# Kernel optimization log

Hardware: AMD Instinct MI355X
Metric: run time of the kernel (lower is better)

The kernel has to match this reference:

```python
import jax, jax.numpy as jnp
import numpy as np

K = 5  # Chebyshev order


def laplacian(w):
    # normalized Laplacian: I - D^{-1/2} W D^{-1/2}
    d = jnp.sum(w, axis=1)
    d_re = 1.0 / jnp.sqrt(d + 1e-5)
    return jnp.eye(w.shape[0], dtype=w.dtype) - d_re[:, None] * w * d_re[None, :]


def cheb_terms(x, lap, k):
    # x: [B,N,C], lap: [N,N] -> [B,k,N,C]
    # Faithful to torch code: T0 = ones, then (x, lap@x) recurrence for k>2.
    t0 = jnp.ones_like(x)
    if k == 1:
        return t0[:, None]
    t1 = jnp.matmul(lap, x)
    if k == 2:
        return jnp.stack([t0, t1], axis=1)
    terms = [t0, x, t1]
    tkm1, tk = x, t1
    for _ in range(3, k):
        tkm1, tk = tk, 2.0 * jnp.matmul(lap, tk) - tkm1
        terms.append(tk)
    return jnp.stack(terms, axis=1)


def graph_conv(x, lap, w, k):
    # torch: cp.permute(0,2,3,1).flatten(2) @ w, i.e. flat index = c*k + t
    t = cheb_terms(x, lap, k)                       # [B,k,N,C]
    C = x.shape[-1]
    O = w.shape[-1]
    return jnp.einsum('bknc,cko->bno', t, w.reshape(C, k, O))


def setup_inputs() -> dict:
    key = jax.random.key(0)
    ks = jax.random.split(key, 9)
    B, N, Cin, H = 8192, 32, 60, 128
    return {
        'x': jax.random.normal(ks[0], (B, N, Cin), dtype=jnp.float32),
        'adj': jax.random.normal(ks[1], (N, N), dtype=jnp.float32) * 0.1,
        'adj_bias': jax.random.normal(ks[2], (1,), dtype=jnp.float32) * 0.1 + 0.2,
        'w1': jax.random.normal(ks[3], (K * Cin, H), dtype=jnp.float32) * 0.05,
        'b1': jax.random.normal(ks[4], (1, 1, H), dtype=jnp.float32) * 0.05,
        'w2': jax.random.normal(ks[5], (K * H, H), dtype=jnp.float32) * 0.05,
        'b2': jax.random.normal(ks[6], (1, 1, H), dtype=jnp.float32) * 0.05,
        'fc_w': jax.random.normal(ks[7], (2, N * H), dtype=jnp.float32) * 0.02,
        'fc_b': jax.random.normal(ks[8], (2,), dtype=jnp.float32) * 0.02,
    }


def reference(x, adj, adj_bias, w1, b1, w2, b2, fc_w, fc_b):
    # DGCNN.forward (eval mode: dropout = identity)
    a = jax.nn.relu(adj + adj_bias)
    lap = laplacian(a)
    h = graph_conv(x, lap, w1, K)
    h = jax.nn.relu(h + b1)      # B1ReLU
    h = graph_conv(h, lap, w2, K)
    h = jax.nn.relu(h + b2)
    h = h.reshape(h.shape[0], -1)  # [B, N*H]
    return h @ fc_w.T + fc_b
```

## Files before the change

### kernel.cpp

```cpp
#include <hip/hip_runtime.h>

typedef unsigned short u16;
typedef unsigned int u32;
typedef short bf16x8 __attribute__((ext_vector_type(8)));
typedef float f32x4 __attribute__((ext_vector_type(4)));

#define MFMA16(a, b, c) __builtin_amdgcn_mfma_f32_16x16x32_bf16((a), (b), (c), 0, 0, 0)

__device__ __forceinline__ u16 f2bf(float f) {
  u32 u = __builtin_bit_cast(u32, f);
  u += 0x7FFFu + ((u >> 16) & 1u);
  return (u16)(u >> 16);
}
__device__ __forceinline__ u32 pk2bf(float a, float b) {
#if __has_builtin(__builtin_amdgcn_cvt_pk_bf16_f32)
  auto v = __builtin_amdgcn_cvt_pk_bf16_f32(a, b);
  return __builtin_bit_cast(u32, v);
#else
  return (u32)f2bf(a) | ((u32)f2bf(b) << 16);
#endif
}

#define WS_MGF   0
#define WS_WT1F  8192
#define WS_WT2F  73728
#define WS_B1    204800
#define WS_B2    205312

__global__ void prep_kernel(const float* __restrict__ adj,
                            const float* __restrict__ adj_bias,
                            const float* __restrict__ w1,
                            const float* __restrict__ b1,
                            const float* __restrict__ w2,
                            const float* __restrict__ b2,
                            char* __restrict__ ws) {
  const int tid = threadIdx.x;
  if (blockIdx.x == 0) {
    __shared__ float sa[1024], Ls[1024], L2s[1024], L3s[1024], sdre[32];
    float bias = adj_bias[0];
    for (int i = tid; i < 1024; i += 256) sa[i] = fmaxf(adj[i] + bias, 0.0f);
    __syncthreads();
    if (tid < 32) {
      float s = 0.0f;
      for (int c = 0; c < 32; ++c) s += sa[tid * 32 + c];
      sdre[tid] = 1.0f / sqrtf(s + 1e-5f);
    }
    __syncthreads();
    for (int i = tid; i < 1024; i += 256) {
      int n = i >> 5, c = i & 31;
      Ls[i] = (n == c ? 1.0f : 0.0f) - sdre[n] * sa[i] * sdre[c];
    }
    __syncthreads();
    for (int i = tid; i < 1024; i += 256) {
      int r = i >> 5, c = i & 31;
      float s = 0.0f;
      for (int m = 0; m < 32; ++m) s += Ls[r * 32 + m] * Ls[m * 32 + c];
      L2s[i] = s;
    }
    __syncthreads();
    for (int i = tid; i < 1024; i += 256) {
      int r = i >> 5, c = i & 31;
      float s = 0.0f;
      for (int m = 0; m < 32; ++m) s += L2s[r * 32 + m] * Ls[m * 32 + c];
      L3s[i] = s;
    }
    __syncthreads();
    u16* MGf = (u16*)(ws + WS_MGF);
    for (int i = tid; i < 4096; i += 256) {
      int jt = i >> 9, lane = (i >> 3) & 63, j = i & 7;
      int col = jt * 16 + (lane & 15);
      int k = ((lane >> 4) << 3) + j;
      int kk = col >> 5, np = col & 31;
      float v;
      if (kk == 0)      v = (np == k) ? 1.0f : 0.0f;
      else if (kk == 1) v = Ls[np * 32 + k];
      else if (kk == 2) v = 2.0f * L2s[np * 32 + k] - (np == k ? 1.0f : 0.0f);
      else              v = 4.0f * L3s[np * 32 + k] - 3.0f * Ls[np * 32 + k];
      MGf[i] = f2bf(v);
    }
    float* B1 = (float*)(ws + WS_B1);
    float* B2 = (float*)(ws + WS_B2);
    if (tid < 128) {
      float s = b1[tid];
      for (int c = 0; c < 60; ++c) s += w1[(c * 5) * 128 + tid];
      B1[tid] = s;
    } else {
      int o = tid - 128;
      float s = b2[o];
      for (int c = 0; c < 128; ++c) s += w2[(c * 5) * 128 + o];
      B2[o] = s;
    }
  } else {
    u16* WT1F = (u16*)(ws + WS_WT1F);
    u16* WT2F = (u16*)(ws + WS_WT2F);
    int g = (blockIdx.x - 1) * 256 + tid;
    for (int i = g; i < 32768; i += 16 * 256) {
      int j = i & 7, lane = (i >> 3) & 63, ks = (i >> 9) & 3;
      int h = (i >> 11) & 1, ot = i >> 12;
      int q = lane >> 4;
      int c = h * 32 + q * 8 + j;
      int o = ot * 16 + (lane & 15);
      WT1F[i] = (c < 60) ? f2bf(w1[(c * 5 + ks + 1) * 128 + o]) : (u16)0;
    }
    for (int i = g; i < 65536; i += 16 * 256) {
      int j = i & 7, lane = (i >> 3) & 63, ks = (i >> 9) & 3;
      int h = (i >> 11) & 3, mt = i >> 13;
      int q = lane >> 4;
      int c2 = h * 32 + q * 8 + j;
      int o = mt * 16 + (lane & 15);
      WT2F[i] = f2bf(w2[(c2 * 5 + ks + 1) * 128 + o]);
    }
  }
}

__global__ __launch_bounds__(256, 4) void dgcnn_kernel(
    const float* __restrict__ x,
    const char* __restrict__ ws,
    const float* __restrict__ fc_w,
    const float* __restrict__ fc_b,
    float* __restrict__ out) {
  __shared__ __align__(16) char arena[35840];
  __shared__ float red[16];
  u16* XtA = (u16*)arena;
  u16* XtB = (u16*)(arena + 5120);
  u16* HtA = (u16*)arena;
  u16* HtB = (u16*)(arena + 9216);
  u16* YA  = (u16*)(arena + 18432);
  u16* YB  = (u16*)(arena + 27136);

  const u16* MGf  = (const u16*)(ws + WS_MGF);
  const u16* WT1F = (const u16*)(ws + WS_WT1F);
  const u16* WT2F = (const u16*)(ws + WS_WT2F);
  const float* bias1 = (const float*)(ws + WS_B1);
  const float* bias2 = (const float*)(ws + WS_B2);

  const int tid = threadIdx.x;
  const int w = tid >> 6, lane = tid & 63;
  const int l15 = lane & 15, q = lane >> 4;
  const int b0 = blockIdx.x * 2;
  const f32x4 z4 = {0.0f, 0.0f, 0.0f, 0.0f};

  bf16x8 mB0 = *(const bf16x8*)(MGf + ((2 * w + 0) * 64 + lane) * 8);
  bf16x8 mB1 = *(const bf16x8*)(MGf + ((2 * w + 1) * 64 + lane) * 8);

  for (int i = tid; i < 160; i += 256) {
    int r = 60 + i / 40, c = i % 40;
    XtA[r * 40 + c] = 0;
    XtB[r * 40 + c] = 0;
  }
  const float* xb = x + (size_t)b0 * 1920;
  for (int i = tid; i < 1920; i += 256) {
    int n = i / 60, c = i - n * 60;
    u32 p = pk2bf(xb[i], xb[1920 + i]);
    XtA[c * 40 + n] = (u16)p;
    XtB[c * 40 + n] = (u16)(p >> 16);
  }
  __syncthreads();

  f32x4 acc1A[2][2] = {{z4, z4}, {z4, z4}};
  f32x4 acc1B[2][2] = {{z4, z4}, {z4, z4}};
#pragma unroll
  for (int h = 0; h < 2; ++h) {
    {
      f32x4 gA[2][2], gB[2][2];
#pragma unroll
      for (int mtl = 0; mtl < 2; ++mtl) {
        int roff = ((2 * h + mtl) * 16 + l15) * 40 + q * 8;
        bf16x8 aA = *(const bf16x8*)&XtA[roff];
        bf16x8 aB = *(const bf16x8*)&XtB[roff];
        gA[mtl][0] = MFMA16(aA, mB0, z4);
        gA[mtl][1] = MFMA16(aA, mB1, z4);
        gB[mtl][0] = MFMA16(aB, mB0, z4);
        gB[mtl][1] = MFMA16(aB, mB1, z4);
      }
#pragma unroll
      for (int mtl = 0; mtl < 2; ++mtl)
#pragma unroll
        for (int jtl = 0; jtl < 2; ++jtl) {
          int np = jtl * 16 + l15;
          int off = np * 136 + w * 32 + mtl * 16 + q * 4;
          uint2 vA, vB;
          vA.x = pk2bf(gA[mtl][jtl][0], gA[mtl][jtl][1]);
          vA.y = pk2bf(gA[mtl][jtl][2], gA[mtl][jtl][3]);
          vB.x = pk2bf(gB[mtl][jtl][0], gB[mtl][jtl][1]);
          vB.y = pk2bf(gB[mtl][jtl][2], gB[mtl][jtl][3]);
          *(uint2*)&YA[off] = vA;
          *(uint2*)&YB[off] = vB;
        }
    }
    __syncthreads();
#pragma unroll
    for (int ks = 0; ks < 4; ++ks) {
      bf16x8 wfa = *(const bf16x8*)(WT1F + ((((2 * w + 0) * 2 + h) * 4 + ks) * 64 + lane) * 8);
      bf16x8 wfb = *(const bf16x8*)(WT1F + ((((2 * w + 1) * 2 + h) * 4 + ks) * 64 + lane) * 8);
      int yoff = ks * 32 + q * 8;
      bf16x8 a0A = *(const bf16x8*)&YA[l15 * 136 + yoff];
      bf16x8 a1A = *(const bf16x8*)&YA[(16 + l15) * 136 + yoff];
      bf16x8 a0B = *(const bf16x8*)&YB[l15 * 136 + yoff];
      bf16x8 a1B = *(const bf16x8*)&YB[(16 + l15) * 136 + yoff];
      acc1A[0][0] = MFMA16(a0A, wfa, acc1A[0][0]);
      acc1A[0][1] = MFMA16(a0A, wfb, acc1A[0][1]);
      acc1A[1][0] = MFMA16(a1A, wfa, acc1A[1][0]);
      acc1A[1][1] = MFMA16(a1A, wfb, acc1A[1][1]);
      acc1B[0][0] = MFMA16(a0B, wfa, acc1B[0][0]);
      acc1B[0][1] = MFMA16(a0B, wfb, acc1B[0][1]);
      acc1B[1][0] = MFMA16(a1B, wfa, acc1B[1][0]);
      acc1B[1][1] = MFMA16(a1B, wfb, acc1B[1][1]);
    }
    if (h == 0) __syncthreads();
  }
#pragma unroll
  for (int ot = 0; ot < 2; ++ot) {
    int o = (2 * w + ot) * 16 + l15;
    float bv = bias1[o];
#pragma unroll
    for (int mt = 0; mt < 2; ++mt) {
      int off = o * 36 + mt * 16 + q * 4;
      uint2 vA, vB;
      vA.x = pk2bf(fmaxf(acc1A[mt][ot][0] + bv, 0.0f), fmaxf(acc1A[mt][ot][1] + bv, 0.0f));
      vA.y = pk2bf(fmaxf(acc1A[mt][ot][2] + bv, 0.0f), fmaxf(acc1A[mt][ot][3] + bv, 0.0f));
      vB.x = pk2bf(fmaxf(acc1B[mt][ot][0] + bv, 0.0f), fmaxf(acc1B[mt][ot][1] + bv, 0.0f));
      vB.y = pk2bf(fmaxf(acc1B[mt][ot][2] + bv, 0.0f), fmaxf(acc1B[mt][ot][3] + bv, 0.0f));
      *(uint2*)&HtA[off] = vA;
      *(uint2*)&HtB[off] = vB;
    }
  }
  __syncthreads();

  f32x4 acc2A[2][2] = {{z4, z4}, {z4, z4}};
  f32x4 acc2B[2][2] = {{z4, z4}, {z4, z4}};
#pragma unroll
  for (int h = 0; h < 4; ++h) {
    {
      f32x4 gA[2][2], gB[2][2];
#pragma unroll
      for (int mtl = 0; mtl < 2; ++mtl) {
        int roff = ((2 * h + mtl) * 16 + l15) * 36 + q * 8;
        bf16x8 aA = *(const bf16x8*)&HtA[roff];
        bf16x8 aB = *(const bf16x8*)&HtB[roff];
        gA[mtl][0] = MFMA16(aA, mB0, z4);
        gA[mtl][1] = MFMA16(aA, mB1, z4);
        gB[mtl][0] = MFMA16(aB, mB0, z4);
        gB[mtl][1] = MFMA16(aB, mB1, z4);
      }
#pragma unroll
      for (int mtl = 0; mtl < 2; ++mtl)
#pragma unroll
        for (int jtl = 0; jtl < 2; ++jtl) {
          int np = jtl * 16 + l15;
          int off = np * 136 + w * 32 + mtl * 16 + q * 4;
          uint2 vA, vB;
          vA.x = pk2bf(gA[mtl][jtl][0], gA[mtl][jtl][1]);
          vA.y = pk2bf(gA[mtl][jtl][2], gA[mtl][jtl][3]);
          vB.x = pk2bf(gB[mtl][jtl][0], gB[mtl][jtl][1]);
          vB.y = pk2bf(gB[mtl][jtl][2], gB[mtl][jtl][3]);
          *(uint2*)&YA[off] = vA;
          *(uint2*)&YB[off] = vB;
        }
    }
    __syncthreads();
#pragma unroll
    for (int ks = 0; ks < 4; ++ks) {
      bf16x8 wfa = *(const bf16x8*)(WT2F + ((((2 * w + 0) * 4 + h) * 4 + ks) * 64 + lane) * 8);
      bf16x8 wfb = *(const bf16x8*)(WT2F + ((((2 * w + 1) * 4 + h) * 4 + ks) * 64 + lane) * 8);
      int yoff = ks * 32 + q * 8;
      bf16x8 by0A = *(const bf16x8*)&YA[l15 * 136 + yoff];
      bf16x8 by1A = *(const bf16x8*)&YA[(16 + l15) * 136 + yoff];
      bf16x8 by0B = *(const bf16x8*)&YB[l15 * 136 + yoff];
      bf16x8 by1B = *(const bf16x8*)&YB[(16 + l15) * 136 + yoff];
      acc2A[0][0] = MFMA16(wfa, by0A, acc2A[0][0]);
      acc2A[0][1] = MFMA16(wfa, by1A, acc2A[0][1]);
      acc2A[1][0] = MFMA16(wfb, by0A, acc2A[1][0]);
      acc2A[1][1] = MFMA16(wfb, by1A, acc2A[1][1]);
      acc2B[0][0] = MFMA16(wfa, by0B, acc2B[0][0]);
      acc2B[0][1] = MFMA16(wfa, by1B, acc2B[0][1]);
      acc2B[1][0] = MFMA16(wfb, by0B, acc2B[1][0]);
      acc2B[1][1] = MFMA16(wfb, by1B, acc2B[1][1]);
    }
    if (h < 3) __syncthreads();
  }

  float p0A = 0.0f, p1A = 0.0f, p0B = 0.0f, p1B = 0.0f;
#pragma unroll
  for (int ot = 0; ot < 2; ++ot) {
    int ob = (2 * w + ot) * 16 + q * 4;
    float4 bv = *(const float4*)&bias2[ob];
#pragma unroll
    for (int nt = 0; nt < 2; ++nt) {
      int n = nt * 16 + l15;
      float4 w0 = *(const float4*)&fc_w[n * 128 + ob];
      float4 w1v = *(const float4*)&fc_w[4096 + n * 128 + ob];
      float hA0 = fmaxf(acc2A[ot][nt][0] + bv.x, 0.0f);
      float hA1 = fmaxf(acc2A[ot][nt][1] + bv.y, 0.0f);
      float hA2 = fmaxf(acc2A[ot][nt][2] + bv.z, 0.0f);
      float hA3 = fmaxf(acc2A[ot][nt][3] + bv.w, 0.0f);
      float hB0 = fmaxf(acc2B[ot][nt][0] + bv.x, 0.0f);
      float hB1 = fmaxf(acc2B[ot][nt][1] + bv.y, 0.0f);
      float hB2 = fmaxf(acc2B[ot][nt][2] + bv.z, 0.0f);
      float hB3 = fmaxf(acc2B[ot][nt][3] + bv.w, 0.0f);
      p0A = fmaf(hA0, w0.x, fmaf(hA1, w0.y, fmaf(hA2, w0.z, fmaf(hA3, w0.w, p0A))));
      p1A = fmaf(hA0, w1v.x, fmaf(hA1, w1v.y, fmaf(hA2, w1v.z, fmaf(hA3, w1v.w, p1A))));
      p0B = fmaf(hB0, w0.x, fmaf(hB1, w0.y, fmaf(hB2, w0.z, fmaf(hB3, w0.w, p0B))));
      p1B = fmaf(hB0, w1v.x, fmaf(hB1, w1v.y, fmaf(hB2, w1v.z, fmaf(hB3, w1v.w, p1B))));
    }
  }
#pragma unroll
  for (int off = 32; off >= 1; off >>= 1) {
    p0A += __shfl_xor(p0A, off);
    p1A += __shfl_xor(p1A, off);
    p0B += __shfl_xor(p0B, off);
    p1B += __shfl_xor(p1B, off);
  }
  if (lane == 0) {
    red[w * 4 + 0] = p0A;
    red[w * 4 + 1] = p1A;
    red[w * 4 + 2] = p0B;
    red[w * 4 + 3] = p1B;
  }
  __syncthreads();
  if (tid < 4) {
    float s = red[tid] + red[4 + tid] + red[8 + tid] + red[12 + tid] + fc_b[tid & 1];
    out[(b0 + (tid >> 1)) * 2 + (tid & 1)] = s;
  }
}

extern "C" void kernel_launch(void* const* d_in, const int* in_sizes, int n_in,
                              void* d_out, int out_size, void* d_ws, size_t ws_size,
                              hipStream_t stream) {
  const float* x        = (const float*)d_in[0];
  const float* adj      = (const float*)d_in[1];
  const float* adj_bias = (const float*)d_in[2];
  const float* w1       = (const float*)d_in[3];
  const float* b1       = (const float*)d_in[4];
  const float* w2       = (const float*)d_in[5];
  const float* b2       = (const float*)d_in[6];
  const float* fc_w     = (const float*)d_in[7];
  const float* fc_b     = (const float*)d_in[8];
  float* out = (float*)d_out;
  char* ws   = (char*)d_ws;

  prep_kernel<<<17, 256, 0, stream>>>(adj, adj_bias, w1, b1, w2, b2, ws);
  dgcnn_kernel<<<4096, 256, 0, stream>>>(x, ws, fc_w, fc_b, out);
}
```

Baseline: 192.6 us.

## Double-buffer Y staging to overlap Chebyshev expansion with weight GEMM

Adds a second pair of Y staging buffers in shared memory. The graph-propagation step for chunk h+1 can then be written while the weight GEMM for chunk h reads the other buffer, and the number of barriers per layer drops from two per chunk to one. In exchange, LDS per block grows from about 35 KB to about 53 KB and the launch-bounds occupancy hint is lowered from 4 to 3 blocks per CU, which may reduce latency hiding across blocks.

```diff
diff --git a/kernel.cpp b/kernel.cpp
--- a/kernel.cpp
+++ b/kernel.cpp
@@ -113,20 +113,22 @@
   }
 }
 
-__global__ __launch_bounds__(256, 4) void dgcnn_kernel(
+__global__ __launch_bounds__(256, 3) void dgcnn_kernel(
     const float* __restrict__ x,
     const char* __restrict__ ws,
     const float* __restrict__ fc_w,
     const float* __restrict__ fc_b,
     float* __restrict__ out) {
-  __shared__ __align__(16) char arena[35840];
+  __shared__ __align__(16) char arena[53248];
   __shared__ float red[16];
   u16* XtA = (u16*)arena;
   u16* XtB = (u16*)(arena + 5120);
   u16* HtA = (u16*)arena;
   u16* HtB = (u16*)(arena + 9216);
-  u16* YA  = (u16*)(arena + 18432);
-  u16* YB  = (u16*)(arena + 27136);
+  u16* Y0A = (u16*)(arena + 18432);
+  u16* Y0B = (u16*)(arena + 27136);
+  u16* Y1A = (u16*)(arena + 35840);
+  u16* Y1B = (u16*)(arena + 44544);
 
   const u16* MGf  = (const u16*)(ws + WS_MGF);
   const u16* WT1F = (const u16*)(ws + WS_WT1F);
@@ -155,49 +157,47 @@
     XtA[c * 40 + n] = (u16)p;
     XtB[c * 40 + n] = (u16)(p >> 16);
   }
-  __syncthreads();
 
   f32x4 acc1A[2][2] = {{z4, z4}, {z4, z4}};
   f32x4 acc1B[2][2] = {{z4, z4}, {z4, z4}};
-#pragma unroll
-  for (int h = 0; h < 2; ++h) {
-    {
-      f32x4 gA[2][2], gB[2][2];
-#pragma unroll
-      for (int mtl = 0; mtl < 2; ++mtl) {
-        int roff = ((2 * h + mtl) * 16 + l15) * 40 + q * 8;
-        bf16x8 aA = *(const bf16x8*)&XtA[roff];
-        bf16x8 aB = *(const bf16x8*)&XtB[roff];
-        gA[mtl][0] = MFMA16(aA, mB0, z4);
-        gA[mtl][1] = MFMA16(aA, mB1, z4);
-        gB[mtl][0] = MFMA16(aB, mB0, z4);
-        gB[mtl][1] = MFMA16(aB, mB1, z4);
+
+  auto G1L1 = [&](int h, u16* Ya, u16* Yb) {
+    f32x4 gA[2][2], gB[2][2];
+#pragma unroll
+    for (int mtl = 0; mtl < 2; ++mtl) {
+      int roff = ((2 * h + mtl) * 16 + l15) * 40 + q * 8;
+      bf16x8 aA = *(const bf16x8*)&XtA[roff];
+      bf16x8 aB = *(const bf16x8*)&XtB[roff];
+      gA[mtl][0] = MFMA16(aA, mB0, z4);
+      gA[mtl][1] = MFMA16(aA, mB1, z4);
+      gB[mtl][0] = MFMA16(aB, mB0, z4);
+      gB[mtl][1] = MFMA16(aB, mB1, z4);
+    }
+#pragma unroll
+    for (int mtl = 0; mtl < 2; ++mtl)
+#pragma unroll
+      for (int jtl = 0; jtl < 2; ++jtl) {
+        int np = jtl * 16 + l15;
+        int off = np * 136 + w * 32 + mtl * 16 + q * 4;
+        uint2 vA, vB;
+        vA.x = pk2bf(gA[mtl][jtl][0], gA[mtl][jtl][1]);
+        vA.y = pk2bf(gA[mtl][jtl][2], gA[mtl][jtl][3]);
+        vB.x = pk2bf(gB[mtl][jtl][0], gB[mtl][jtl][1]);
+        vB.y = pk2bf(gB[mtl][jtl][2], gB[mtl][jtl][3]);
+        *(uint2*)&Ya[off] = vA;
+        *(uint2*)&Yb[off] = vB;
       }
-#pragma unroll
-      for (int mtl = 0; mtl < 2; ++mtl)
-#pragma unroll
-        for (int jtl = 0; jtl < 2; ++jtl) {
-          int np = jtl * 16 + l15;
-          int off = np * 136 + w * 32 + mtl * 16 + q * 4;
-          uint2 vA, vB;
-          vA.x = pk2bf(gA[mtl][jtl][0], gA[mtl][jtl][1]);
-          vA.y = pk2bf(gA[mtl][jtl][2], gA[mtl][jtl][3]);
-          vB.x = pk2bf(gB[mtl][jtl][0], gB[mtl][jtl][1]);
-          vB.y = pk2bf(gB[mtl][jtl][2], gB[mtl][jtl][3]);
-          *(uint2*)&YA[off] = vA;
-          *(uint2*)&YB[off] = vB;
-        }
-    }
-    __syncthreads();
+  };
+  auto E1 = [&](int h, const u16* Ya, const u16* Yb) {
 #pragma unroll
     for (int ks = 0; ks < 4; ++ks) {
       bf16x8 wfa = *(const bf16x8*)(WT1F + ((((2 * w + 0) * 2 + h) * 4 + ks) * 64 + lane) * 8);
       bf16x8 wfb = *(const bf16x8*)(WT1F + ((((2 * w + 1) * 2 + h) * 4 + ks) * 64 + lane) * 8);
       int yoff = ks * 32 + q * 8;
-      bf16x8 a0A = *(const bf16x8*)&YA[l15 * 136 + yoff];
-      bf16x8 a1A = *(const bf16x8*)&YA[(16 + l15) * 136 + yoff];
-      bf16x8 a0B = *(const bf16x8*)&YB[l15 * 136 + yoff];
-      bf16x8 a1B = *(const bf16x8*)&YB[(16 + l15) * 136 + yoff];
+      bf16x8 a0A = *(const bf16x8*)&Ya[l15 * 136 + yoff];
+      bf16x8 a1A = *(const bf16x8*)&Ya[(16 + l15) * 136 + yoff];
+      bf16x8 a0B = *(const bf16x8*)&Yb[l15 * 136 + yoff];
+      bf16x8 a1B = *(const bf16x8*)&Yb[(16 + l15) * 136 + yoff];
       acc1A[0][0] = MFMA16(a0A, wfa, acc1A[0][0]);
       acc1A[0][1] = MFMA16(a0A, wfb, acc1A[0][1]);
       acc1A[1][0] = MFMA16(a1A, wfa, acc1A[1][0]);
@@ -207,8 +207,15 @@
       acc1B[1][0] = MFMA16(a1B, wfa, acc1B[1][0]);
       acc1B[1][1] = MFMA16(a1B, wfb, acc1B[1][1]);
     }
-    if (h == 0) __syncthreads();
-  }
+  };
+
+  __syncthreads();
+  G1L1(0, Y0A, Y0B);
+  __syncthreads();
+  G1L1(1, Y1A, Y1B);
+  E1(0, Y0A, Y0B);
+  __syncthreads();
+  E1(1, Y1A, Y1B);
 #pragma unroll
   for (int ot = 0; ot < 2; ++ot) {
     int o = (2 * w + ot) * 16 + l15;
@@ -229,45 +236,44 @@
 
   f32x4 acc2A[2][2] = {{z4, z4}, {z4, z4}};
   f32x4 acc2B[2][2] = {{z4, z4}, {z4, z4}};
-#pragma unroll
-  for (int h = 0; h < 4; ++h) {
-    {
-      f32x4 gA[2][2], gB[2][2];
-#pragma unroll
-      for (int mtl = 0; mtl < 2; ++mtl) {
-        int roff = ((2 * h + mtl) * 16 + l15) * 36 + q * 8;
-        bf16x8 aA = *(const bf16x8*)&HtA[roff];
-        bf16x8 aB = *(const bf16x8*)&HtB[roff];
-        gA[mtl][0] = MFMA16(aA, mB0, z4);
-        gA[mtl][1] = MFMA16(aA, mB1, z4);
-        gB[mtl][0] = MFMA16(aB, mB0, z4);
-        gB[mtl][1] = MFMA16(aB, mB1, z4);
+
+  auto G1L2 = [&](int h, u16* Ya, u16* Yb) {
+    f32x4 gA[2][2], gB[2][2];
+#pragma unroll
+    for (int mtl = 0; mtl < 2; ++mtl) {
+      int roff = ((2 * h + mtl) * 16 + l15) * 36 + q * 8;
+      bf16x8 aA = *(const bf16x8*)&HtA[roff];
+      bf16x8 aB = *(const bf16x8*)&HtB[roff];
+      gA[mtl][0] = MFMA16(aA, mB0, z4);
+      gA[mtl][1] = MFMA16(aA, mB1, z4);
+      gB[mtl][0] = MFMA16(aB, mB0, z4);
+      gB[mtl][1] = MFMA16(aB, mB1, z4);
+    }
+#pragma unroll
+    for (int mtl = 0; mtl < 2; ++mtl)
+#pragma unroll
+      for (int jtl = 0; jtl < 2; ++jtl) {
+        int np = jtl * 16 + l15;
+        int off = np * 136 + w * 32 + mtl * 16 + q * 4;
+        uint2 vA, vB;
+        vA.x = pk2bf(gA[mtl][jtl][0], gA[mtl][jtl][1]);
+        vA.y = pk2bf(gA[mtl][jtl][2], gA[mtl][jtl][3]);
+        vB.x = pk2bf(gB[mtl][jtl][0], gB[mtl][jtl][1]);
+        vB.y = pk2bf(gB[mtl][jtl][2], gB[mtl][jtl][3]);
+        *(uint2*)&Ya[off] = vA;
+        *(uint2*)&Yb[off] = vB;
       }
-#pragma unroll
-      for (int mtl = 0; mtl < 2; ++mtl)
-#pragma unroll
-        for (int jtl = 0; jtl < 2; ++jtl) {
-          int np = jtl * 16 + l15;
-          int off = np * 136 + w * 32 + mtl * 16 + q * 4;
-          uint2 vA, vB;
-          vA.x = pk2bf(gA[mtl][jtl][0], gA[mtl][jtl][1]);
-          vA.y = pk2bf(gA[mtl][jtl][2], gA[mtl][jtl][3]);
-          vB.x = pk2bf(gB[mtl][jtl][0], gB[mtl][jtl][1]);
-          vB.y = pk2bf(gB[mtl][jtl][2], gB[mtl][jtl][3]);
-          *(uint2*)&YA[off] = vA;
-          *(uint2*)&YB[off] = vB;
-        }
-    }
-    __syncthreads();
+  };
+  auto E2 = [&](int h, const u16* Ya, const u16* Yb) {
 #pragma unroll
     for (int ks = 0; ks < 4; ++ks) {
       bf16x8 wfa = *(const bf16x8*)(WT2F + ((((2 * w + 0) * 4 + h) * 4 + ks) * 64 + lane) * 8);
       bf16x8 wfb = *(const bf16x8*)(WT2F + ((((2 * w + 1) * 4 + h) * 4 + ks) * 64 + lane) * 8);
       int yoff = ks * 32 + q * 8;
-      bf16x8 by0A = *(const bf16x8*)&YA[l15 * 136 + yoff];
-      bf16x8 by1A = *(const bf16x8*)&YA[(16 + l15) * 136 + yoff];
-      bf16x8 by0B = *(const bf16x8*)&YB[l15 * 136 + yoff];
-      bf16x8 by1B = *(const bf16x8*)&YB[(16 + l15) * 136 + yoff];
+      bf16x8 by0A = *(const bf16x8*)&Ya[l15 * 136 + yoff];
+      bf16x8 by1A = *(const bf16x8*)&Ya[(16 + l15) * 136 + yoff];
+      bf16x8 by0B = *(const bf16x8*)&Yb[l15 * 136 + yoff];
+      bf16x8 by1B = *(const bf16x8*)&Yb[(16 + l15) * 136 + yoff];
       acc2A[0][0] = MFMA16(wfa, by0A, acc2A[0][0]);
       acc2A[0][1] = MFMA16(wfa, by1A, acc2A[0][1]);
       acc2A[1][0] = MFMA16(wfb, by0A, acc2A[1][0]);
@@ -277,8 +283,20 @@
       acc2B[1][0] = MFMA16(wfb, by0B, acc2B[1][0]);
       acc2B[1][1] = MFMA16(wfb, by1B, acc2B[1][1]);
     }
-    if (h < 3) __syncthreads();
-  }
+  };
+
+  G1L2(0, Y0A, Y0B);
+  __syncthreads();
+  G1L2(1, Y1A, Y1B);
+  E2(0, Y0A, Y0B);
+  __syncthreads();
+  G1L2(2, Y0A, Y0B);
+  E2(1, Y1A, Y1B);
+  __syncthreads();
+  G1L2(3, Y1A, Y1B);
+  E2(2, Y0A, Y0B);
+  __syncthreads();
+  E2(3, Y1A, Y1B);
 
   float p0A = 0.0f, p1A = 0.0f, p0B = 0.0f, p1B = 0.0f;
 #pragma unroll
```

Result: slower. 207.5 us (+7.7%).
